# Kernel tuning notes

Measured on AMD Instinct MI355X. Metric: run time of the kernel, lower is better.

## Reference

```python
import jax, jax.numpy as jnp
import numpy as np

HEADS = 16
HEAD_DIM = 64
DIM = HEADS * HEAD_DIM          # 1024
TEXT_LEN = 226
N_CONCEPTS = 8
FRAMES = 4
PATCHES = 16 * 24               # H*W per latent frame
IMG_LEN = FRAMES * PATCHES      # 1536
TIME_DIM = 512
FF_DIM = 4 * DIM
TOPK_HEADS = 4                  # imap_sep_topk
LN_EPS = 1e-5
QK_EPS = 1e-6


def _layer_norm(x, w, b, eps):
    mu = jnp.mean(x, -1, keepdims=True)
    var = jnp.var(x, -1, keepdims=True)
    return (x - mu) * jax.lax.rsqrt(var + eps) * w + b


def _norm_zero(h, e, temb, lw, lb, nw, nb):
    # CogVideoXLayerNormZero: adaLN shift/scale/gate for hidden and encoder streams
    s = jax.nn.silu(temb) @ lw + lb                      # [B, 6*DIM]
    shift, scale, gate, e_shift, e_scale, e_gate = jnp.split(s, 6, axis=1)
    hn = _layer_norm(h, nw, nb, LN_EPS) * (1 + scale)[:, None] + shift[:, None]
    en = _layer_norm(e, nw, nb, LN_EPS) * (1 + e_scale)[:, None] + e_shift[:, None]
    return hn, en, gate[:, None], e_gate[:, None]


def _heads(x):
    B, S, _ = x.shape
    return x.reshape(B, S, HEADS, HEAD_DIM).transpose(0, 2, 1, 3)


def _rope(x, cos, sin):
    # diffusers apply_rotary_emb, use_real_unbind_dim=-1
    xr = x.reshape(*x.shape[:-1], HEAD_DIM // 2, 2)
    rot = jnp.stack([-xr[..., 1], xr[..., 0]], -1).reshape(x.shape)
    return x * cos + rot * sin


def _sdpa(q, k, v):
    s = jnp.einsum('bhqd,bhkd->bhqk', q, k) * (1.0 / np.sqrt(HEAD_DIM))
    return jnp.einsum('bhqk,bhkd->bhqd', jax.nn.softmax(s, -1), v)


def _attention(norm_h, norm_e, norm_c, rope_cos, rope_sin,
               wq, wk, wv, nq_w, nq_b, nk_w, nk_b, wo, bo):
    B = norm_h.shape[0]
    hs = jnp.concatenate([norm_e, norm_h], axis=1)       # [B, T+P, DIM]
    q, k, v = _heads(hs @ wq), _heads(hs @ wk), _heads(hs @ wv)
    cq, ck, cv = _heads(norm_c @ wq), _heads(norm_c @ wk), _heads(norm_c @ wv)
    q = _layer_norm(q, nq_w, nq_b, QK_EPS); cq = _layer_norm(cq, nq_w, nq_b, QK_EPS)
    k = _layer_norm(k, nk_w, nk_b, QK_EPS); ck = _layer_norm(ck, nk_w, nk_b, QK_EPS)
    q = q.at[:, :, TEXT_LEN:].set(_rope(q[:, :, TEXT_LEN:], rope_cos, rope_sin))
    k = k.at[:, :, TEXT_LEN:].set(_rope(k[:, :, TEXT_LEN:], rope_cos, rope_sin))

    attn_out = _sdpa(q, k, v)                            # [B,H,S,D]
    img_hidden = attn_out[:, :, TEXT_LEN:]               # [B,H,IMG_LEN,D]

    # select_head (reconstructed): per-head spread of image-token activations, top-k heads
    head_score = jnp.std(jnp.mean(img_hidden[1], -1), -1)        # [H]
    _, sel_head_idx = jax.lax.top_k(head_score, TOPK_HEADS)

    iq, ik, iv = q[:, :, TEXT_LEN:], k[:, :, TEXT_LEN:], v[:, :, TEXT_LEN:]
    cat_q = jnp.concatenate([cq, iq], 2)
    cat_k = jnp.concatenate([ck, ik], 2)
    cat_v = jnp.concatenate([cv, iv], 2)
    concept_attn = _sdpa(cat_q, cat_k, cat_v)
    attn_concept = concept_attn[:, :, :N_CONCEPTS]       # [B,H,C,D]

    cross_maps = jnp.mean(jnp.einsum('hpd,hcd->hcp', iq[1], ck[1]), axis=0)
    concept_maps = jnp.sum(jnp.einsum('hcd,hpd->hcp', attn_concept[1], img_hidden[1]), axis=0)

    # select_visual_token (reconstructed): per (head, concept, frame) argmax patch of q.k sim
    text_key = ck[1]                                      # imap_qk_matching_target == 'concept'
    sim = jnp.einsum('hpd,htd->htp', iq[1], text_key).reshape(HEADS, N_CONCEPTS, FRAMES, PATCHES)
    sel_vis_idx = jnp.argmax(sim, axis=-1)                # [H,T,F]

    img_r = img_hidden[1].reshape(HEADS, FRAMES, PATCHES, HEAD_DIM)
    h_ix = jnp.arange(HEADS)[:, None, None]
    f_ix = jnp.arange(FRAMES)[None, None, :]
    sel_img = img_r[h_ix, f_ix, sel_vis_idx]              # [H,T,F,D] gather
    imap = jnp.einsum('htfd,hfpd->htfp', sel_img, img_r)
    imap = (imap - imap.mean(1, keepdims=True)) / (jnp.std(imap, axis=1, keepdims=True, ddof=1) + 1e-6)
    imap = imap.reshape(HEADS, N_CONCEPTS, FRAMES * PATCHES)
    sel_imap = jnp.mean(imap[sel_head_idx], axis=0)       # [T, F*P]
    imap_sum = jnp.sum(imap, axis=0)

    def merge(x):
        return x.transpose(0, 2, 1, 3).reshape(B, x.shape[2], DIM)

    out = merge(attn_out) @ wo + bo
    c_out = merge(attn_concept) @ wo + bo
    return out[:, TEXT_LEN:], out[:, :TEXT_LEN], c_out, sel_imap, imap_sum, concept_maps, cross_maps


def _ff(x, w1, b1, w2, b2):
    return jax.nn.gelu(x @ w1 + b1, approximate=True) @ w2 + b2


def _block(hidden_states, encoder_hidden_states, concept_hidden_states, temb,
           rope_cos, rope_sin,
           norm1_w, norm1_b, ln1_w, ln1_b, norm2_w, norm2_b, ln2_w, ln2_b,
           wq, wk, wv, nq_w, nq_b, nk_w, nk_b, wo, bo,
           ff_w1, ff_b1, ff_w2, ff_b2):
    h, e, c = hidden_states, encoder_hidden_states, concept_hidden_states
    nh, ne, g_msa, eg_msa = _norm_zero(h, e, temb, norm1_w, norm1_b, ln1_w, ln1_b)
    _, nc, _, cg_msa = _norm_zero(h, c, temb, norm1_w, norm1_b, ln1_w, ln1_b)

    a_h, a_e, a_c, sel_imap, imap, concept_maps, cross_maps = _attention(
        nh, ne, nc, rope_cos, rope_sin, wq, wk, wv, nq_w, nq_b, nk_w, nk_b, wo, bo)

    h = h + g_msa * a_h
    e = e + eg_msa * a_e
    c = c + cg_msa * a_c

    nh, ne, g_ff, eg_ff = _norm_zero(h, e, temb, norm2_w, norm2_b, ln2_w, ln2_b)
    _, nc, _, cg_ff = _norm_zero(h, c, temb, norm2_w, norm2_b, ln2_w, ln2_b)

    ff_out = _ff(jnp.concatenate([ne, nh], axis=1), ff_w1, ff_b1, ff_w2, ff_b2)
    ff_c = _ff(nc, ff_w1, ff_b1, ff_w2, ff_b2)
    h = h + g_ff * ff_out[:, TEXT_LEN:]
    e = e + eg_ff * ff_out[:, :TEXT_LEN]
    c = c + cg_ff * ff_c
    return h, e, c, sel_imap, imap, concept_maps, cross_maps


def setup_inputs():
    key = jax.random.key(0)
    ks = jax.random.split(key, 16)
    p = lambda i, shape: jax.random.normal(ks[i], shape, jnp.float32) * 0.02
    return dict(
        hidden_states=jax.random.normal(ks[0], (2, IMG_LEN, DIM), jnp.float32),
        encoder_hidden_states=jax.random.normal(ks[1], (2, TEXT_LEN, DIM), jnp.float32),
        concept_hidden_states=jax.random.normal(ks[2], (2, N_CONCEPTS, DIM), jnp.float32),
        temb=jax.random.normal(ks[3], (2, TIME_DIM), jnp.float32),
        rope_cos=jax.random.uniform(ks[4], (IMG_LEN, HEAD_DIM), jnp.float32),
        rope_sin=jax.random.uniform(ks[5], (IMG_LEN, HEAD_DIM), jnp.float32),
        norm1_w=p(6, (TIME_DIM, 6 * DIM)), norm1_b=jnp.zeros((6 * DIM,), jnp.float32),
        ln1_w=jnp.ones((DIM,), jnp.float32), ln1_b=jnp.zeros((DIM,), jnp.float32),
        norm2_w=p(7, (TIME_DIM, 6 * DIM)), norm2_b=jnp.zeros((6 * DIM,), jnp.float32),
        ln2_w=jnp.ones((DIM,), jnp.float32), ln2_b=jnp.zeros((DIM,), jnp.float32),
        wq=p(8, (DIM, DIM)), wk=p(9, (DIM, DIM)), wv=p(10, (DIM, DIM)),
        nq_w=jnp.ones((HEAD_DIM,), jnp.float32), nq_b=jnp.zeros((HEAD_DIM,), jnp.float32),
        nk_w=jnp.ones((HEAD_DIM,), jnp.float32), nk_b=jnp.zeros((HEAD_DIM,), jnp.float32),
        wo=p(11, (DIM, DIM)), bo=jnp.zeros((DIM,), jnp.float32),
        ff_w1=p(12, (DIM, FF_DIM)), ff_b1=jnp.zeros((FF_DIM,), jnp.float32),
        ff_w2=p(13, (FF_DIM, DIM)), ff_b2=jnp.zeros((DIM,), jnp.float32),
    )


def reference(hidden_states, encoder_hidden_states, concept_hidden_states, temb,
              rope_cos, rope_sin,
              norm1_w, norm1_b, ln1_w, ln1_b, norm2_w, norm2_b, ln2_w, ln2_b,
              wq, wk, wv, nq_w, nq_b, nk_w, nk_b, wo, bo,
              ff_w1, ff_b1, ff_w2, ff_b2):
    return _block(hidden_states, encoder_hidden_states, concept_hidden_states, temb,
                  rope_cos, rope_sin,
                  norm1_w, norm1_b, ln1_w, ln1_b, norm2_w, norm2_b, ln2_w, ln2_b,
                  wq, wk, wv, nq_w, nq_b, nk_w, nk_b, wo, bo,
                  ff_w1, ff_b1, ff_w2, ff_b2)
```

## Files before the change

### kernel.cpp

```cpp
#include <hip/hip_runtime.h>
#include <hip/hip_bf16.h>
#include <math.h>

#define B_ 2
#define HEADS_ 16
#define HD_ 64
#define DIM_ 1024
#define TEXT_ 226
#define NC_ 8
#define FRAMES_ 4
#define PATCHES_ 384
#define IMG_ 1536
#define S_MAIN 1762
#define S2_ 1770
#define TD_ 512
#define FF_ 4096
#define ROWS_ (B_*S2_)
#define VPAD_ 1792

#define OFF_S1   0L
#define OFF_S2   12288L
#define OFF_MISC 24576L
#define OFF_SIM  25600L
#define OFF_IMAP 222208L
#define OFF_AC   418816L
#define OFF_X    435200L
#define OFF_PROJ 4060160L
#define OFF_XN   7685120L
#define OFF_Q    11310080L
#define OFF_K    14935040L
#define OFF_V    18560000L
#define OFF_AO   22184960L
#define OFF_XNB  25809920L

#define O_H    0L
#define O_E    3145728L
#define O_C    3608576L
#define O_SELI 3624960L
#define O_ISUM 3637248L
#define O_CMAP 3649536L
#define O_XMAP 3661824L

typedef __bf16 bf16x8_t __attribute__((ext_vector_type(8)));
typedef float  f32x4_t  __attribute__((ext_vector_type(4)));

__device__ __forceinline__ unsigned int pack2bf(float a, float b) {
    unsigned short ua = __builtin_bit_cast(unsigned short, (__bf16)a);
    unsigned short ub = __builtin_bit_cast(unsigned short, (__bf16)b);
    return (unsigned int)ua | ((unsigned int)ub << 16);
}

__device__ __forceinline__ void stage16(const unsigned short* g, unsigned short* l) {
    __builtin_amdgcn_global_load_lds(
        (const __attribute__((address_space(1))) unsigned int*)g,
        (__attribute__((address_space(3))) unsigned int*)l, 16, 0, 0);
}

__global__ __launch_bounds__(256) void k_silu_mod(
    const float* __restrict__ temb, const float* __restrict__ w1, const float* __restrict__ b1,
    const float* __restrict__ w2, const float* __restrict__ b2,
    float* __restrict__ s1, float* __restrict__ s2)
{
    int gout = blockIdx.x * 64 + (threadIdx.x & 63);
    int ks = threadIdx.x >> 6;
    int which = gout / 12288;
    int r = gout % 12288;
    int b = r / 6144, n = r % 6144;
    const float* w = which ? w2 : w1;
    const float* bb = which ? b2 : b1;
    const float* t = temb + b * TD_;
    float acc = 0.f;
    for (int k = ks*128; k < ks*128 + 128; ++k) {
        float tv = t[k];
        float sv = tv / (1.f + __expf(-tv));
        acc += sv * w[(long)k * 6144 + n];
    }
    __shared__ float red[256];
    red[threadIdx.x] = acc; __syncthreads();
    if (ks == 0) {
        int lt = threadIdx.x;
        float v = red[lt] + red[lt+64] + red[lt+128] + red[lt+192] + bb[n];
        (which ? s2 : s1)[b * 6144 + n] = v;
    }
}

__global__ __launch_bounds__(256) void k_tcvt(
    const float* __restrict__ src, unsigned short* __restrict__ dst, int K, int N)
{
    __shared__ float t[32][33];
    int n0 = blockIdx.x * 32, k0 = blockIdx.y * 32;
    int tx = threadIdx.x & 31, ty = threadIdx.x >> 5;
    #pragma unroll
    for (int i = 0; i < 4; ++i)
        t[ty + 8*i][tx] = src[(size_t)(k0 + ty + 8*i) * N + n0 + tx];
    __syncthreads();
    #pragma unroll
    for (int i = 0; i < 4; ++i) {
        float v = t[tx][ty + 8*i];
        dst[(size_t)(n0 + ty + 8*i) * K + k0 + tx] =
            __builtin_bit_cast(unsigned short, (__bf16)v);
    }
}

__global__ __launch_bounds__(256) void k_tcvt_qkv(
    const float* __restrict__ wq, const float* __restrict__ wk, const float* __restrict__ wv,
    unsigned short* __restrict__ dst)
{
    const float* src = (blockIdx.z == 0) ? wq : (blockIdx.z == 1) ? wk : wv;
    unsigned short* d = dst + (size_t)blockIdx.z * 1024 * 1024;
    __shared__ float t[32][33];
    int n0 = blockIdx.x * 32, k0 = blockIdx.y * 32;
    int tx = threadIdx.x & 31, ty = threadIdx.x >> 5;
    #pragma unroll
    for (int i = 0; i < 4; ++i)
        t[ty + 8*i][tx] = src[(size_t)(k0 + ty + 8*i) * 1024 + n0 + tx];
    __syncthreads();
    #pragma unroll
    for (int i = 0; i < 4; ++i) {
        float v = t[tx][ty + 8*i];
        d[(size_t)(n0 + ty + 8*i) * 1024 + k0 + tx] =
            __builtin_bit_cast(unsigned short, (__bf16)v);
    }
}

__global__ __launch_bounds__(256) void k_vtrans(
    const float* __restrict__ vh, unsigned short* __restrict__ vb)
{
    int bh = blockIdx.z;
    int d0 = blockIdx.y * 32;
    int s0 = blockIdx.x * 32;
    __shared__ float t[32][33];
    int tx = threadIdx.x & 31, ty = threadIdx.x >> 5;
    const float* src = vh + (size_t)bh * S2_ * 64;
    #pragma unroll
    for (int i = 0; i < 4; ++i) {
        int s = s0 + ty + 8*i; if (s >= S2_) s = S2_ - 1;
        t[ty + 8*i][tx] = src[(size_t)s*64 + d0 + tx];
    }
    __syncthreads();
    unsigned short* dst = vb + (size_t)bh * 64 * VPAD_;
    #pragma unroll
    for (int i = 0; i < 4; ++i) {
        int d = d0 + ty + 8*i;
        dst[(size_t)d * VPAD_ + s0 + tx] =
            __builtin_bit_cast(unsigned short, (__bf16)t[tx][ty + 8*i]);
    }
}

__global__ __launch_bounds__(256) void k_ln_mod(
    const float* pe, long bse, const float* ph, long bsh, const float* pc, long bsc,
    const float* __restrict__ smod, const float* __restrict__ lnw, const float* __restrict__ lnb,
    float* __restrict__ out, unsigned short* __restrict__ outb)
{
    long row = blockIdx.x;
    int b = (int)(row / S2_), s = (int)(row % S2_);
    const float* src; int shiftB, scaleB;
    if (s < TEXT_)       { src = pe + (long)b*bse + (long)s*DIM_;          shiftB = 3072; scaleB = 4096; }
    else if (s < S_MAIN) { src = ph + (long)b*bsh + (long)(s-TEXT_)*DIM_;  shiftB = 0;    scaleB = 1024; }
    else                 { src = pc + (long)b*bsc + (long)(s-S_MAIN)*DIM_; shiftB = 3072; scaleB = 4096; }
    int tid = threadIdx.x;
    int col = tid * 4;
    float4 x = *(const float4*)(src + col);
    float lsum = x.x + x.y + x.z + x.w;
    float lsq  = x.x*x.x + x.y*x.y + x.z*x.z + x.w*x.w;
    __shared__ float r1[256], r2[256];
    r1[tid] = lsum; r2[tid] = lsq; __syncthreads();
    for (int st = 128; st; st >>= 1) {
        if (tid < st) { r1[tid] += r1[tid+st]; r2[tid] += r2[tid+st]; }
        __syncthreads();
    }
    float mu = r1[0] * (1.f / DIM_);
    float var = r2[0] * (1.f / DIM_) - mu * mu;
    float rstd = rsqrtf(var + 1e-5f);
    const float* sb = smod + (long)b * 6144;
    float xs[4] = {x.x, x.y, x.z, x.w};
    float res[4];
    #pragma unroll
    for (int i = 0; i < 4; ++i) {
        int cc = col + i;
        float yy = (xs[i] - mu) * rstd * lnw[cc] + lnb[cc];
        res[i] = yy * (1.f + sb[scaleB + cc]) + sb[shiftB + cc];
    }
    if (out)
        *(float4*)(out + row * DIM_ + col) = make_float4(res[0], res[1], res[2], res[3]);
    uint2 pk;
    pk.x = pack2bf(res[0], res[1]); pk.y = pack2bf(res[2], res[3]);
    *(uint2*)(outb + row * DIM_ + col) = pk;
}

__global__ __launch_bounds__(256, 4) void k_bgemm(
    const unsigned short* __restrict__ A, const unsigned short* __restrict__ Wt,
    const float* __restrict__ bias, float* __restrict__ out_f,
    unsigned short* __restrict__ out_b, int M, int N, int K, int kz_len, int mode,
    float* __restrict__ q_out, float* __restrict__ k_out, float* __restrict__ v_out)
{
    __shared__ unsigned short at[2][128*32];
    __shared__ unsigned short bt[2][128*32];
    int tid = threadIdx.x;
    int w = tid >> 6, lane = tid & 63;
    int lr = lane & 15, lh = lane >> 4;
    int wm = w >> 1, wn = w & 1;
    int m0 = blockIdx.y * 128, n0 = blockIdx.x * 128;
    int kbeg = blockIdx.z * kz_len, kend = kbeg + kz_len;

    f32x4_t acc[4][4];
    #pragma unroll
    for (int i = 0; i < 4; ++i)
        #pragma unroll
        for (int j = 0; j < 4; ++j) { acc[i][j][0]=0.f; acc[i][j][1]=0.f; acc[i][j][2]=0.f; acc[i][j][3]=0.f; }

    int r4 = tid >> 2, c4 = tid & 3;
    int arow0 = m0 + r4;      if (arow0 >= M) arow0 = M - 1;
    int arow1 = m0 + 64 + r4; if (arow1 >= M) arow1 = M - 1;
    const unsigned short* ga0 = A + (size_t)arow0 * K + c4 * 8;
    const unsigned short* ga1 = A + (size_t)arow1 * K + c4 * 8;
    const unsigned short* gb0 = Wt + (size_t)(n0 + r4) * K + c4 * 8;
    const unsigned short* gb1 = Wt + (size_t)(n0 + 64 + r4) * K + c4 * 8;
    int lbase = w * 512;

    stage16(ga0 + kbeg, &at[0][lbase]);
    stage16(ga1 + kbeg, &at[0][lbase + 2048]);
    stage16(gb0 + kbeg, &bt[0][lbase]);
    stage16(gb1 + kbeg, &bt[0][lbase + 2048]);
    __syncthreads();
    int buf = 0;
    for (int k0 = kbeg; k0 < kend; k0 += 32) {
        bool more = (k0 + 32) < kend;
        if (more) {
            int nb = buf ^ 1;
            stage16(ga0 + k0 + 32, &at[nb][lbase]);
            stage16(ga1 + k0 + 32, &at[nb][lbase + 2048]);
            stage16(gb0 + k0 + 32, &bt[nb][lbase]);
            stage16(gb1 + k0 + 32, &bt[nb][lbase + 2048]);
        }
        int4 af[4], bf[4];
        #pragma unroll
        for (int tm = 0; tm < 4; ++tm)
            af[tm] = *(const int4*)&at[buf][(wm*64 + tm*16 + lr)*32 + lh*8];
        #pragma unroll
        for (int tn = 0; tn < 4; ++tn)
            bf[tn] = *(const int4*)&bt[buf][(wn*64 + tn*16 + lr)*32 + lh*8];
        #pragma unroll
        for (int tm = 0; tm < 4; ++tm) {
            bf16x8_t av = __builtin_bit_cast(bf16x8_t, af[tm]);
            #pragma unroll
            for (int tn = 0; tn < 4; ++tn)
                acc[tm][tn] = __builtin_amdgcn_mfma_f32_16x16x32_bf16(
                    av, __builtin_bit_cast(bf16x8_t, bf[tn]), acc[tm][tn], 0, 0, 0);
        }
        __syncthreads();
        buf ^= 1;
    }
    float* of = out_f;
    if (mode == 1) of += (size_t)blockIdx.z * M * N;
    #pragma unroll
    for (int tm = 0; tm < 4; ++tm) {
        #pragma unroll
        for (int r = 0; r < 4; ++r) {
            int m = m0 + wm*64 + tm*16 + lh*4 + r;
            if (m >= M) continue;
            int b = m / S2_, s = m % S2_;
            #pragma unroll
            for (int tn = 0; tn < 4; ++tn) {
                int n = n0 + wn*64 + tn*16 + lr;
                float v = acc[tm][tn][r];
                if (mode == 0) {
                    int which = n >> 10, c = n & 1023;
                    int hh = c >> 6, d = c & 63;
                    float* dstp = (which == 0) ? q_out : (which == 1) ? k_out : v_out;
                    dstp[(((size_t)b*HEADS_ + hh)*S2_ + s)*64 + d] = v;
                } else if (mode == 1) {
                    of[(size_t)m * N + n] = v + (bias ? bias[n] : 0.f);
                } else {
                    float x = v + bias[n];
                    float u = 0.7978845608028654f * (x + 0.044715f*x*x*x);
                    float g = x / (1.f + __expf(-2.f*u));
                    out_b[(size_t)m * N + n] = __builtin_bit_cast(unsigned short, (__bf16)g);
                }
            }
        }
    }
}

__global__ __launch_bounds__(256) void k_gemm(
    const float* __restrict__ A, const float* __restrict__ W,
    float* __restrict__ C, int M, int N, int K, int kz_len, int headed, int row_off,
    float* __restrict__ part)
{
    __shared__ float As[16][68];
    __shared__ float Bs[16][68];
    int tid = threadIdx.x;
    int bm = blockIdx.y * 64, bn = blockIdx.x * 64;
    int tr = tid >> 4, tc = tid & 15;
    int ar = tid >> 2, akk = (tid & 3) * 4;
    int bkk = tid >> 4, bn4 = (tid & 15) * 4;
    float acc[4][4] = {{0.f}};
    int garow = bm + ar;
    const float* Aptr = A + (size_t)garow * K + akk;
    const float* Wptr = W + (size_t)bkk * N + bn + bn4;
    int kbeg = blockIdx.z * kz_len;
    for (int k0 = kbeg; k0 < kbeg + kz_len; k0 += 16) {
        float4 av = make_float4(0.f, 0.f, 0.f, 0.f);
        if (garow < M) av = *(const float4*)(Aptr + k0);
        As[akk+0][ar] = av.x; As[akk+1][ar] = av.y; As[akk+2][ar] = av.z; As[akk+3][ar] = av.w;
        float4 bv = *(const float4*)(Wptr + (size_t)k0 * N);
        Bs[bkk][bn4+0] = bv.x; Bs[bkk][bn4+1] = bv.y; Bs[bkk][bn4+2] = bv.z; Bs[bkk][bn4+3] = bv.w;
        __syncthreads();
        #pragma unroll
        for (int kk = 0; kk < 16; ++kk) {
            float4 a = *(const float4*)&As[kk][tr*4];
            float4 bq = *(const float4*)&Bs[kk][tc*4];
            float avv[4] = {a.x, a.y, a.z, a.w};
            float bvv[4] = {bq.x, bq.y, bq.z, bq.w};
            #pragma unroll
            for (int i = 0; i < 4; ++i)
                #pragma unroll
                for (int j = 0; j < 4; ++j)
                    acc[i][j] += avv[i] * bvv[j];
        }
        __syncthreads();
    }
    #pragma unroll
    for (int i = 0; i < 4; ++i) {
        int r = bm + tr*4 + i;
        if (r >= M) continue;
        #pragma unroll
        for (int j = 0; j < 4; ++j) {
            int n = bn + tc*4 + j;
            float v = acc[i][j];
            if (part) {
                part[(size_t)blockIdx.z*M*N + (size_t)r*N + n] = v;
            } else if (headed) {
                int rg = r + row_off;
                int b = rg / S2_, s = rg % S2_;
                int hh = n >> 6, d = n & 63;
                C[(((size_t)b*HEADS_ + hh)*S2_ + s)*64 + d] = v;
            } else {
                C[(size_t)(r + row_off) * N + n] = v;
            }
        }
    }
}

__global__ __launch_bounds__(256) void k_fixred(
    const float* __restrict__ pa, float* __restrict__ qh_out)
{
    long i = (long)blockIdx.x*256 + threadIdx.x;
    int r = (int)(i >> 10), n = (int)(i & 1023);
    float v = pa[i] + pa[i + (long)IMG_*DIM_];
    int hh = n >> 6, d = n & 63;
    qh_out[(((size_t)HEADS_ + hh)*S2_ + TEXT_ + r)*64 + d] = v;
}

__global__ __launch_bounds__(256) void k_qk_prep(
    float* qh, float* kh, unsigned short* qbb, unsigned short* kbb,
    const float* __restrict__ nqw, const float* __restrict__ nqb,
    const float* __restrict__ nkw, const float* __restrict__ nkb,
    const float* __restrict__ rc, const float* __restrict__ rs)
{
    int which = blockIdx.y;
    int wid = threadIdx.x >> 6;
    int lane = threadIdx.x & 63;
    long row = (long)blockIdx.x * 4 + wid;
    long s = row % S2_;
    bool b1 = row >= (long)HEADS_*S2_;
    float* base = (which ? kh : qh) + row * 64;
    const float* w  = which ? nkw : nqw;
    const float* bb = which ? nkb : nqb;
    float x = base[lane];
    float sum = x;
    for (int off = 1; off < 64; off <<= 1) sum += __shfl_xor(sum, off, 64);
    float mu = sum * (1.f / 64.f);
    float dx = x - mu;
    float v = dx * dx;
    for (int off = 1; off < 64; off <<= 1) v += __shfl_xor(v, off, 64);
    float rstd = rsqrtf(v * (1.f / 64.f) + 1e-6f);
    float y = dx * rstd * w[lane] + bb[lane];
    if (s >= TEXT_ && s < S_MAIN) {
        long p = s - TEXT_;
        float part = __shfl_xor(y, 1, 64);
        float rot = (lane & 1) ? part : -part;
        y = y * rc[p*64 + lane] + rot * rs[p*64 + lane];
    }
    bool needf = b1 && (which ? (s >= S_MAIN) : (s >= TEXT_ && s < S_MAIN));
    if (needf) base[lane] = y;
    (which ? kbb : qbb)[row * 64 + lane] = __builtin_bit_cast(unsigned short, (__bf16)y);
}

__global__ __launch_bounds__(256) void k_flash(
    const unsigned short* __restrict__ qb, const unsigned short* __restrict__ kb,
    const unsigned short* __restrict__ vb,
    float* __restrict__ p0, float* __restrict__ p1, float* __restrict__ pl)
{
    int bx = blockIdx.x;
    int h = blockIdx.y, b = blockIdx.z;
    int qt, NQ, q_off, r0s, r0e, r1s, r1e, z;
    if (bx < 28) {
        z = bx & 1; int u = bx >> 1;
        qt = u*128; NQ = S_MAIN; q_off = 0;
        r0s = z ? 896 : 0; r0e = z ? S_MAIN : 896;
        r1s = 0; r1e = 0;
    } else {
        z = bx - 28;
        qt = 0; NQ = NC_; q_off = S_MAIN;
        if (z == 0) { r0s = S_MAIN;      r0e = S2_;    r1s = TEXT_; r1e = TEXT_ + 768; }
        else        { r0s = TEXT_ + 768; r0e = S_MAIN; r1s = 0;     r1e = 0; }
    }
    float* po = z ? p1 : p0;
    int tid = threadIdx.x;
    int w = tid >> 6, lane = tid & 63;
    int lr = lane & 15, lh = lane >> 4;
    __shared__ __align__(16) unsigned short kt[64*72];
    __shared__ __align__(16) unsigned short vt[64*72];
    __shared__ __align__(16) unsigned short pbuf[4*32*72];
    unsigned short* pw = pbuf + w*32*72;
    const unsigned short* qbase = qb + (((size_t)b*HEADS_ + h)*S2_ + q_off)*64;
    const unsigned short* kbase = kb + ((size_t)b*HEADS_ + h)*S2_*64;
    const unsigned short* vbase = vb + (size_t)(b*HEADS_ + h)*64*VPAD_;
    bf16x8_t aq[2][2];
    #pragma unroll
    for (int t = 0; t < 2; ++t) {
        int qrow = qt + w*32 + t*16 + lr; if (qrow >= NQ) qrow = NQ - 1;
        const unsigned short* qsrc = qbase + (size_t)qrow*64 + lh*8;
        aq[t][0] = __builtin_bit_cast(bf16x8_t, *(const int4*)qsrc);
        aq[t][1] = __builtin_bit_cast(bf16x8_t, *(const int4*)(qsrc + 32));
    }
    int4 onesi = make_int4(0x3F803F80, 0x3F803F80, 0x3F803F80, 0x3F803F80);
    bf16x8_t bones = __builtin_bit_cast(bf16x8_t, onesi);
    f32x4_t O[2][4];
    f32x4_t Lacc[2];
    #pragma unroll
    for (int t = 0; t < 2; ++t) {
        Lacc[t][0]=0.f; Lacc[t][1]=0.f; Lacc[t][2]=0.f; Lacc[t][3]=0.f;
        #pragma unroll
        for (int g = 0; g < 4; ++g) { O[t][g][0]=0.f; O[t][g][1]=0.f; O[t][g][2]=0.f; O[t][g][3]=0.f; }
    }
    for (int rgi = 0; rgi < 2; ++rgi) {
        int rs = rgi ? r1s : r0s, re = rgi ? r1e : r0e;
        for (int j0 = rs; j0 < re; j0 += 64) {
            int cnt = min(64, re - j0);
            __syncthreads();
            #pragma unroll
            for (int i = 0; i < 2; ++i) {
                int idx = tid + i*256;
                int key = idx >> 3, p8 = idx & 7;
                int krow = j0 + key; if (krow > re - 1) krow = re - 1;
                *(int4*)&kt[key*72 + p8*8] = *(const int4*)(kbase + (size_t)krow*64 + p8*8);
            }
            #pragma unroll
            for (int i = 0; i < 2; ++i) {
                int idx = tid + i*256;
                int d = idx >> 3, p8 = idx & 7;
                *(int4*)&vt[d*72 + p8*8] = *(const int4*)(vbase + (size_t)d*VPAD_ + j0 + p8*8);
            }
            __syncthreads();
            f32x4_t S[2][4];
            #pragma unroll
            for (int g = 0; g < 4; ++g) {
                const unsigned short* kr = &kt[(16*g + lr)*72 + lh*8];
                bf16x8_t b0 = __builtin_bit_cast(bf16x8_t, *(const int4*)kr);
                bf16x8_t b1 = __builtin_bit_cast(bf16x8_t, *(const int4*)(kr + 32));
                #pragma unroll
                for (int t = 0; t < 2; ++t) {
                    f32x4_t zz; zz[0]=0.f; zz[1]=0.f; zz[2]=0.f; zz[3]=0.f;
                    zz = __builtin_amdgcn_mfma_f32_16x16x32_bf16(aq[t][0], b0, zz, 0, 0, 0);
                    zz = __builtin_amdgcn_mfma_f32_16x16x32_bf16(aq[t][1], b1, zz, 0, 0, 0);
                    S[t][g] = zz;
                }
            }
            #pragma unroll
            for (int t = 0; t < 2; ++t)
                #pragma unroll
                for (int g = 0; g < 4; ++g) {
                    bool vld = (16*g + lr) < cnt;
                    #pragma unroll
                    for (int r = 0; r < 4; ++r) {
                        float p = vld ? __expf(S[t][g][r] * 0.125f) : 0.f;
                        pw[(t*16 + lh*4 + r)*72 + 16*g + lr] = __builtin_bit_cast(unsigned short, (__bf16)p);
                    }
                }
            #pragma unroll
            for (int c = 0; c < 2; ++c) {
                bf16x8_t ap[2];
                #pragma unroll
                for (int t = 0; t < 2; ++t) {
                    ap[t] = __builtin_bit_cast(bf16x8_t,
                        *(const int4*)&pw[(t*16 + lr)*72 + c*32 + lh*8]);
                    Lacc[t] = __builtin_amdgcn_mfma_f32_16x16x32_bf16(ap[t], bones, Lacc[t], 0, 0, 0);
                }
                #pragma unroll
                for (int g = 0; g < 4; ++g) {
                    bf16x8_t bv = __builtin_bit_cast(bf16x8_t,
                        *(const int4*)&vt[(16*g + lr)*72 + c*32 + lh*8]);
                    #pragma unroll
                    for (int t = 0; t < 2; ++t)
                        O[t][g] = __builtin_amdgcn_mfma_f32_16x16x32_bf16(ap[t], bv, O[t][g], 0, 0, 0);
                }
            }
        }
    }
    #pragma unroll
    for (int t = 0; t < 2; ++t)
        #pragma unroll
        for (int r = 0; r < 4; ++r) {
            int gq = qt + w*32 + t*16 + lh*4 + r;
            if (gq < NQ) {
                long rrow = (long)(b*HEADS_ + h)*S2_ + q_off + gq;
                float* o = po + rrow*64 + lr;
                #pragma unroll
                for (int g = 0; g < 4; ++g) o[16*g] = O[t][g][r];
                if (lr == 0) pl[(long)z*(B_*HEADS_*S2_) + rrow] = Lacc[t][r];
            }
        }
}

__global__ __launch_bounds__(256) void k_fcomb(
    const float* __restrict__ p0, const float* __restrict__ p1,
    const float* __restrict__ pl,
    float* __restrict__ ao, float* __restrict__ ac)
{
    long i = (long)blockIdx.x*256 + threadIdx.x;
    int d = (int)(i & 63);
    long rrow = i >> 6;
    int s = (int)(rrow % S2_);
    int bh = (int)(rrow / S2_);
    float l = pl[rrow] + pl[rrow + (long)B_*HEADS_*S2_];
    float v = (p0[i] + p1[i]) / l;
    if (s < S_MAIN) ao[((long)bh*S_MAIN + s)*64 + d] = v;
    else            ac[((long)bh*NC_ + (s - S_MAIN))*64 + d] = v;
}

__global__ __launch_bounds__(256) void k_head_score(const float* __restrict__ ao, float* __restrict__ score)
{
    int h = blockIdx.x, tid = threadIdx.x;
    const float* base = ao + (((long)HEADS_ + h)*S_MAIN + TEXT_)*64;
    float sA = 0.f, sB = 0.f;
    for (int p = tid; p < IMG_; p += 256) {
        const float* r = base + (long)p*64;
        float mm = 0.f;
        for (int d = 0; d < 64; d += 4) {
            float4 v = *(const float4*)(r + d);
            mm += v.x + v.y + v.z + v.w;
        }
        mm *= (1.f / 64.f);
        sA += mm; sB += mm*mm;
    }
    __shared__ float r1[256], r2[256];
    r1[tid] = sA; r2[tid] = sB; __syncthreads();
    for (int st = 128; st; st >>= 1) {
        if (tid < st) { r1[tid] += r1[tid+st]; r2[tid] += r2[tid+st]; }
        __syncthreads();
    }
    if (tid == 0) {
        float mean = r1[0] / IMG_, ms = r2[0] / IMG_;
        score[h] = sqrtf(fmaxf(ms - mean*mean, 0.f));
    }
}

__global__ void k_top4(const float* __restrict__ score, int* __restrict__ sel)
{
    if (threadIdx.x == 0 && blockIdx.x == 0) {
        int used = 0;
        for (int k = 0; k < 4; ++k) {
            float best = -INFINITY; int bi = 0;
            for (int h2 = 0; h2 < 16; ++h2) {
                if (used & (1 << h2)) continue;
                if (score[h2] > best) { best = score[h2]; bi = h2; }
            }
            used |= 1 << bi; sel[k] = bi;
        }
    }
}

__global__ __launch_bounds__(512) void k_sim(
    const float* __restrict__ qh, const float* __restrict__ kh,
    float* __restrict__ sim, int* __restrict__ selvis)
{
    int blk = blockIdx.x;
    int h = blk >> 5, t = (blk >> 2) & 7, f = blk & 3;
    int tid = threadIdx.x;
    __shared__ float ckv[64];
    if (tid < 64) ckv[tid] = kh[(((long)HEADS_ + h)*S2_ + S_MAIN + t)*64 + tid];
    __syncthreads();
    float val = -INFINITY; int idx = 0x7fffffff;
    if (tid < PATCHES_) {
        const float* qrow = qh + (((long)HEADS_ + h)*S2_ + TEXT_ + f*PATCHES_ + tid)*64;
        float acc = 0.f;
        for (int d = 0; d < 64; d += 4) {
            float4 qv = *(const float4*)(qrow + d);
            acc += qv.x*ckv[d] + qv.y*ckv[d+1] + qv.z*ckv[d+2] + qv.w*ckv[d+3];
        }
        sim[((long)h*NC_ + t)*IMG_ + f*PATCHES_ + tid] = acc;
        val = acc; idx = tid;
    }
    __shared__ float sv[512]; __shared__ int si[512];
    sv[tid] = val; si[tid] = idx; __syncthreads();
    for (int st = 256; st; st >>= 1) {
        if (tid < st) {
            float v2 = sv[tid+st]; int i2 = si[tid+st];
            if (v2 > sv[tid] || (v2 == sv[tid] && i2 < si[tid])) { sv[tid] = v2; si[tid] = i2; }
        }
        __syncthreads();
    }
    if (tid == 0) selvis[blk] = si[0];
}

__global__ __launch_bounds__(256) void k_cross(const float* __restrict__ sim, float* __restrict__ out)
{
    int i = blockIdx.x*256 + threadIdx.x;
    int c = i / IMG_, p = i % IMG_;
    float acc = 0.f;
    for (int h = 0; h < 16; ++h) acc += sim[((long)h*NC_ + c)*IMG_ + p];
    out[O_XMAP + i] = acc * (1.f / 16.f);
}

__global__ __launch_bounds__(256) void k_concept_maps(
    const float* __restrict__ ac, const float* __restrict__ ao, float* __restrict__ out)
{
    int i = blockIdx.x*256 + threadIdx.x;
    int c = i / IMG_, p = i % IMG_;
    float acc = 0.f;
    for (int h = 0; h < 16; ++h) {
        const float* a = ac + (((long)HEADS_ + h)*NC_ + c)*64;
        const float* g = ao + (((long)HEADS_ + h)*S_MAIN + TEXT_ + p)*64;
        for (int d = 0; d < 64; d += 4) {
            float4 av = *(const float4*)(a + d);
            float4 gv = *(const float4*)(g + d);
            acc += av.x*gv.x + av.y*gv.y + av.z*gv.z + av.w*gv.w;
        }
    }
    out[O_CMAP + i] = acc;
}

__global__ void k_imap_raw(const float* __restrict__ ao, const int* __restrict__ selvis,
                           float* __restrict__ imap)
{
    int blk = blockIdx.x;
    int h = blk >> 5, t = (blk >> 2) & 7, f = blk & 3;
    int tid = threadIdx.x;
    __shared__ float sel[64];
    int pstar = selvis[blk];
    if (tid < 64) sel[tid] = ao[(((long)HEADS_ + h)*S_MAIN + TEXT_ + f*PATCHES_ + pstar)*64 + tid];
    __syncthreads();
    const float* g = ao + (((long)HEADS_ + h)*S_MAIN + TEXT_ + f*PATCHES_ + tid)*64;
    float acc = 0.f;
    for (int d = 0; d < 64; d += 4) {
        float4 gv = *(const float4*)(g + d);
        acc += gv.x*sel[d] + gv.y*sel[d+1] + gv.z*sel[d+2] + gv.w*sel[d+3];
    }
    imap[((long)h*NC_ + t)*IMG_ + f*PATCHES_ + tid] = acc;
}

__global__ __launch_bounds__(256) void k_imap_norm(float* __restrict__ imap)
{
    int i = blockIdx.x*256 + threadIdx.x;
    int h = i / IMG_, fp = i % IMG_;
    float v[8]; float mu = 0.f;
    #pragma unroll
    for (int t = 0; t < 8; ++t) { v[t] = imap[((long)h*NC_ + t)*IMG_ + fp]; mu += v[t]; }
    mu *= 0.125f;
    float var = 0.f;
    #pragma unroll
    for (int t = 0; t < 8; ++t) var += (v[t]-mu)*(v[t]-mu);
    float sd = sqrtf(var * (1.f / 7.f));
    float inv = 1.f / (sd + 1e-6f);
    #pragma unroll
    for (int t = 0; t < 8; ++t) imap[((long)h*NC_ + t)*IMG_ + fp] = (v[t]-mu)*inv;
}

__global__ __launch_bounds__(256) void k_imap_reduce(
    const float* __restrict__ imap, const int* __restrict__ sel, float* __restrict__ out)
{
    int i = blockIdx.x*256 + threadIdx.x;
    int t = i / IMG_, fp = i % IMG_;
    float sum = 0.f;
    for (int h = 0; h < 16; ++h) sum += imap[((long)h*NC_ + t)*IMG_ + fp];
    float ss = 0.f;
    for (int k = 0; k < 4; ++k) { int h = sel[k]; ss += imap[((long)h*NC_ + t)*IMG_ + fp]; }
    out[O_ISUM + i] = sum;
    out[O_SELI + i] = ss * 0.25f;
}

__global__ __launch_bounds__(256) void k_merge(
    const float* __restrict__ ao, const float* __restrict__ ac, unsigned short* __restrict__ xo)
{
    long i = (long)blockIdx.x*256 + threadIdx.x;
    int col = (int)(i & 1023);
    long row = i >> 10;
    int b = (int)(row / S2_), s = (int)(row % S2_);
    int h = col >> 6, d = col & 63;
    float v;
    if (s < S_MAIN) v = ao[(((long)b*HEADS_ + h)*S_MAIN + s)*64 + d];
    else            v = ac[(((long)b*HEADS_ + h)*NC_ + (s - S_MAIN))*64 + d];
    xo[i] = __builtin_bit_cast(unsigned short, (__bf16)v);
}

__global__ __launch_bounds__(256) void k_residual1(
    const float* __restrict__ pe, const float* __restrict__ ph, const float* __restrict__ pc,
    const float* __restrict__ p0, const float* __restrict__ p1, const float* __restrict__ bo,
    const float* __restrict__ s1, float* __restrict__ X)
{
    long i = (long)blockIdx.x*256 + threadIdx.x;
    int col = (int)(i & 1023);
    long row = i >> 10;
    int b = (int)(row / S2_), s = (int)(row % S2_);
    const float* sb = s1 + (long)b * 6144;
    float orig, gate;
    if (s < TEXT_)       { orig = pe[((long)b*TEXT_ + s)*DIM_ + col];            gate = sb[5120 + col]; }
    else if (s < S_MAIN) { orig = ph[((long)b*IMG_ + (s-TEXT_))*DIM_ + col];     gate = sb[2048 + col]; }
    else                 { orig = pc[((long)b*NC_ + (s-S_MAIN))*DIM_ + col];     gate = sb[5120 + col]; }
    X[i] = orig + gate * (p0[i] + p1[i] + bo[col]);
}

__global__ __launch_bounds__(256) void k_final(
    const float* __restrict__ X, const float* __restrict__ f0, const float* __restrict__ f1,
    const float* __restrict__ fb2, const float* __restrict__ s2, float* __restrict__ out)
{
    long i = (long)blockIdx.x*256 + threadIdx.x;
    int col = (int)(i & 1023);
    long row = i >> 10;
    int b = (int)(row / S2_), s = (int)(row % S2_);
    const float* sb = s2 + (long)b * 6144;
    float gate; float* o;
    if (s < TEXT_)       { gate = sb[5120 + col]; o = out + O_E + ((long)b*TEXT_ + s)*DIM_ + col; }
    else if (s < S_MAIN) { gate = sb[2048 + col]; o = out + O_H + ((long)b*IMG_ + (s-TEXT_))*DIM_ + col; }
    else                 { gate = sb[5120 + col]; o = out + O_C + ((long)b*NC_ + (s-S_MAIN))*DIM_ + col; }
    *o = X[i] + gate * (f0[i] + f1[i] + fb2[col]);
}

extern "C" void kernel_launch(void* const* d_in, const int* in_sizes, int n_in,
                              void* d_out, int out_size, void* d_ws, size_t ws_size,
                              hipStream_t stream)
{
    (void)in_sizes; (void)n_in; (void)out_size; (void)ws_size;
    const float* h_in = (const float*)d_in[0];
    const float* e_in = (const float*)d_in[1];
    const float* c_in = (const float*)d_in[2];
    const float* temb = (const float*)d_in[3];
    const float* rcos = (const float*)d_in[4];
    const float* rsin = (const float*)d_in[5];
    const float* n1w  = (const float*)d_in[6];
    const float* n1b  = (const float*)d_in[7];
    const float* ln1w = (const float*)d_in[8];
    const float* ln1b = (const float*)d_in[9];
    const float* n2w  = (const float*)d_in[10];
    const float* n2b  = (const float*)d_in[11];
    const float* ln2w = (const float*)d_in[12];
    const float* ln2b = (const float*)d_in[13];
    const float* wq   = (const float*)d_in[14];
    const float* wk   = (const float*)d_in[15];
    const float* wv   = (const float*)d_in[16];
    const float* nqw  = (const float*)d_in[17];
    const float* nqb  = (const float*)d_in[18];
    const float* nkw  = (const float*)d_in[19];
    const float* nkb  = (const float*)d_in[20];
    const float* wo   = (const float*)d_in[21];
    const float* bo   = (const float*)d_in[22];
    const float* fw1  = (const float*)d_in[23];
    const float* fb1  = (const float*)d_in[24];
    const float* fw2  = (const float*)d_in[25];
    const float* fb2  = (const float*)d_in[26];

    float* ws  = (float*)d_ws;
    float* out = (float*)d_out;
    float* s1   = ws + OFF_S1;
    float* s2   = ws + OFF_S2;
    float* score  = ws + OFF_MISC;
    int*   selh   = (int*)(ws + OFF_MISC + 16);
    int*   selvis = (int*)(ws + OFF_MISC + 32);
    float* sim  = ws + OFF_SIM;
    float* imap = ws + OFF_IMAP;
    float* ac   = ws + OFF_AC;
    float* X    = ws + OFF_X;
    float* proj = ws + OFF_PROJ;
    float* xn   = ws + OFF_XN;
    float* qh   = ws + OFF_Q;
    float* kh   = ws + OFF_K;
    float* vh   = ws + OFF_V;
    float* ao   = ws + OFF_AO;
    float* ffo  = proj;
    float* fixp = ws + OFF_AO;
    unsigned short* xnb   = (unsigned short*)(ws + OFF_XNB);
    unsigned short* wqkvT = (unsigned short*)(ws + OFF_PROJ);
    unsigned short* vb    = (unsigned short*)(ws + OFF_PROJ);
    unsigned short* qbb   = (unsigned short*)(ws + OFF_X);
    unsigned short* kbb   = qbb + (size_t)B_*HEADS_*S2_*64;
    unsigned short* woT   = (unsigned short*)(ws + OFF_AO + 2000000);
    unsigned short* fw1T  = (unsigned short*)(ws + OFF_V);
    unsigned short* fw2T  = (unsigned short*)(ws + OFF_AO);
    unsigned short* ffh   = (unsigned short*)(ws + OFF_Q);
    float* fp0 = vh;
    float* fp1 = xn;
    float* fpl = sim;

    hipLaunchKernelGGL(k_silu_mod, dim3(384), dim3(256), 0, stream, temb, n1w, n1b, n2w, n2b, s1, s2);
    hipLaunchKernelGGL(k_tcvt_qkv, dim3(32, 32, 3), dim3(256), 0, stream, wq, wk, wv, wqkvT);
    hipLaunchKernelGGL(k_ln_mod, dim3(ROWS_), dim3(256), 0, stream,
        e_in, (long)TEXT_*DIM_, h_in, (long)IMG_*DIM_, c_in, (long)NC_*DIM_, s1, ln1w, ln1b, xn, xnb);
    hipLaunchKernelGGL(k_bgemm, dim3(24, 28, 1), dim3(256), 0, stream,
        xnb, wqkvT, (const float*)nullptr, (float*)nullptr, (unsigned short*)nullptr,
        ROWS_, 3072, 1024, 1024, 0, qh, kh, vh);
    hipLaunchKernelGGL(k_gemm, dim3(16, 24, 2), dim3(256), 0, stream,
        xn + (long)(S2_ + TEXT_)*DIM_, wq, (float*)nullptr, IMG_, DIM_, DIM_, 512, 0, 0, fixp);
    hipLaunchKernelGGL(k_fixred, dim3(6144), dim3(256), 0, stream, fixp, qh);
    hipLaunchKernelGGL(k_gemm, dim3(16, 1, 1), dim3(256), 0, stream,
        xn + (long)(S2_ + S_MAIN)*DIM_, wk, kh, NC_, DIM_, DIM_, 1024, 1, S2_ + S_MAIN, (float*)nullptr);
    hipLaunchKernelGGL(k_qk_prep, dim3(14160, 2), dim3(256), 0, stream,
        qh, kh, qbb, kbb, nqw, nqb, nkw, nkb, rcos, rsin);
    hipLaunchKernelGGL(k_vtrans, dim3(56, 2, 32), dim3(256), 0, stream, vh, vb);
    hipLaunchKernelGGL(k_flash, dim3(30, 16, 2), dim3(256), 0, stream,
        qbb, kbb, vb, fp0, fp1, fpl);
    hipLaunchKernelGGL(k_fcomb, dim3(14160), dim3(256), 0, stream, fp0, fp1, fpl, ao, ac);
    hipLaunchKernelGGL(k_head_score, dim3(16), dim3(256), 0, stream, ao, score);
    hipLaunchKernelGGL(k_top4, dim3(1), dim3(64), 0, stream, score, selh);
    hipLaunchKernelGGL(k_sim, dim3(512), dim3(512), 0, stream, qh, kh, sim, selvis);
    hipLaunchKernelGGL(k_cross, dim3(48), dim3(256), 0, stream, sim, out);
    hipLaunchKernelGGL(k_concept_maps, dim3(48), dim3(256), 0, stream, ac, ao, out);
    hipLaunchKernelGGL(k_imap_raw, dim3(512), dim3(384), 0, stream, ao, selvis, imap);
    hipLaunchKernelGGL(k_imap_norm, dim3(96), dim3(256), 0, stream, imap);
    hipLaunchKernelGGL(k_imap_reduce, dim3(48), dim3(256), 0, stream, imap, selh, out);
    hipLaunchKernelGGL(k_merge, dim3(14160), dim3(256), 0, stream, ao, ac, xnb);
    hipLaunchKernelGGL(k_tcvt, dim3(32, 32), dim3(256), 0, stream, wo, woT, 1024, 1024);
    hipLaunchKernelGGL(k_bgemm, dim3(8, 28, 2), dim3(256), 0, stream,
        xnb, woT, (const float*)nullptr, proj, (unsigned short*)nullptr, ROWS_, DIM_, 1024, 512, 1,
        (float*)nullptr, (float*)nullptr, (float*)nullptr);
    hipLaunchKernelGGL(k_residual1, dim3(14160), dim3(256), 0, stream,
        e_in, h_in, c_in, proj, proj + (size_t)ROWS_*DIM_, bo, s1, X);
    hipLaunchKernelGGL(k_tcvt, dim3(128, 32), dim3(256), 0, stream, fw1, fw1T, 1024, 4096);
    hipLaunchKernelGGL(k_tcvt, dim3(32, 128), dim3(256), 0, stream, fw2, fw2T, 4096, 1024);
    hipLaunchKernelGGL(k_ln_mod, dim3(ROWS_), dim3(256), 0, stream,
        X, (long)S2_*DIM_, X + (long)TEXT_*DIM_, (long)S2_*DIM_, X + (long)S_MAIN*DIM_, (long)S2_*DIM_,
        s2, ln2w, ln2b, (float*)nullptr, xnb);
    hipLaunchKernelGGL(k_bgemm, dim3(32, 28, 1), dim3(256), 0, stream,
        xnb, fw1T, fb1, (float*)nullptr, ffh, ROWS_, FF_, 1024, 1024, 2,
        (float*)nullptr, (float*)nullptr, (float*)nullptr);
    hipLaunchKernelGGL(k_bgemm, dim3(8, 28, 2), dim3(256), 0, stream,
        ffh, fw2T, (const float*)nullptr, ffo, (unsigned short*)nullptr, ROWS_, DIM_, FF_, 2048, 1,
        (float*)nullptr, (float*)nullptr, (float*)nullptr);
    hipLaunchKernelGGL(k_final, dim3(14160), dim3(256), 0, stream,
        X, ffo, ffo + (size_t)ROWS_*DIM_, fb2, s2, out);
}
```

Measured before the change: 734.4 us.

## Swizzle workgroups across XCDs, repad flash LDS, fuse merge into fcomb

Adds an XCD-aware workgroup remapping to the bf16 GEMM, fp32 GEMM and flash kernels so neighbouring tiles land on the same XCD and share L2. Changes the flash kernel's LDS row strides (K/V to 68, P to 76) to change bank-conflict behaviour, and adds a fast path that skips the validity mask when a key tile is full. Removes the separate k_merge kernel by having k_fcomb write the bf16 merged head layout directly, saving one launch and one fp32 re-read. The scattered bf16 writes in fcomb are strided and could be less coalesced than before.

```diff
diff --git a/kernel.cpp b/kernel.cpp
--- a/kernel.cpp
+++ b/kernel.cpp
@@ -41,6 +41,9 @@
 #define O_CMAP 3649536L
 #define O_XMAP 3661824L
 
+#define KS_ 68
+#define PS_ 76
+
 typedef __bf16 bf16x8_t __attribute__((ext_vector_type(8)));
 typedef float  f32x4_t  __attribute__((ext_vector_type(4)));
 
@@ -54,6 +57,11 @@
     __builtin_amdgcn_global_load_lds(
         (const __attribute__((address_space(1))) unsigned int*)g,
         (__attribute__((address_space(3))) unsigned int*)l, 16, 0, 0);
+}
+
+__device__ __forceinline__ int xcd_swz(int lin, int nwg) {
+    if ((nwg & 7) == 0) { int q = nwg >> 3; lin = (lin & 7) * q + (lin >> 3); }
+    return lin;
 }
 
 __global__ __launch_bounds__(256) void k_silu_mod(
@@ -200,7 +208,9 @@
     int w = tid >> 6, lane = tid & 63;
     int lr = lane & 15, lh = lane >> 4;
     int wm = w >> 1, wn = w & 1;
-    int m0 = blockIdx.y * 128, n0 = blockIdx.x * 128;
+    int gx = gridDim.x;
+    int lin = xcd_swz(blockIdx.y * gx + blockIdx.x, gx * gridDim.y);
+    int m0 = (lin / gx) * 128, n0 = (lin % gx) * 128;
     int kbeg = blockIdx.z * kz_len, kend = kbeg + kz_len;
 
     f32x4_t acc[4][4];
@@ -290,7 +300,9 @@
     __shared__ float As[16][68];
     __shared__ float Bs[16][68];
     int tid = threadIdx.x;
-    int bm = blockIdx.y * 64, bn = blockIdx.x * 64;
+    int gx = gridDim.x;
+    int lin = xcd_swz(blockIdx.y * gx + blockIdx.x, gx * gridDim.y);
+    int bm = (lin / gx) * 64, bn = (lin % gx) * 64;
     int tr = tid >> 4, tc = tid & 15;
     int ar = tid >> 2, akk = (tid & 3) * 4;
     int bkk = tid >> 4, bn4 = (tid & 15) * 4;
@@ -392,8 +404,11 @@
     const unsigned short* __restrict__ vb,
     float* __restrict__ p0, float* __restrict__ p1, float* __restrict__ pl)
 {
-    int bx = blockIdx.x;
-    int h = blockIdx.y, b = blockIdx.z;
+    int lin3 = (blockIdx.z * gridDim.y + blockIdx.y) * gridDim.x + blockIdx.x;
+    lin3 = xcd_swz(lin3, gridDim.x * gridDim.y * gridDim.z);
+    int bx = lin3 % 30;
+    int rest = lin3 / 30;
+    int h = rest & 15, b = rest >> 4;
     int qt, NQ, q_off, r0s, r0e, r1s, r1e, z;
     if (bx < 28) {
         z = bx & 1; int u = bx >> 1;
@@ -410,10 +425,10 @@
     int tid = threadIdx.x;
     int w = tid >> 6, lane = tid & 63;
     int lr = lane & 15, lh = lane >> 4;
-    __shared__ __align__(16) unsigned short kt[64*72];
-    __shared__ __align__(16) unsigned short vt[64*72];
-    __shared__ __align__(16) unsigned short pbuf[4*32*72];
-    unsigned short* pw = pbuf + w*32*72;
+    __shared__ __align__(16) unsigned short kt[64*KS_];
+    __shared__ __align__(16) unsigned short vt[64*KS_];
+    __shared__ __align__(16) unsigned short pbuf[4*32*PS_];
+    unsigned short* pw = pbuf + w*32*PS_;
     const unsigned short* qbase = qb + (((size_t)b*HEADS_ + h)*S2_ + q_off)*64;
     const unsigned short* kbase = kb + ((size_t)b*HEADS_ + h)*S2_*64;
     const unsigned short* vbase = vb + (size_t)(b*HEADS_ + h)*64*VPAD_;
@@ -445,19 +460,19 @@
                 int idx = tid + i*256;
                 int key = idx >> 3, p8 = idx & 7;
                 int krow = j0 + key; if (krow > re - 1) krow = re - 1;
-                *(int4*)&kt[key*72 + p8*8] = *(const int4*)(kbase + (size_t)krow*64 + p8*8);
+                *(int4*)&kt[key*KS_ + p8*8] = *(const int4*)(kbase + (size_t)krow*64 + p8*8);
             }
             #pragma unroll
             for (int i = 0; i < 2; ++i) {
                 int idx = tid + i*256;
                 int d = idx >> 3, p8 = idx & 7;
-                *(int4*)&vt[d*72 + p8*8] = *(const int4*)(vbase + (size_t)d*VPAD_ + j0 + p8*8);
+                *(int4*)&vt[d*KS_ + p8*8] = *(const int4*)(vbase + (size_t)d*VPAD_ + j0 + p8*8);
             }
             __syncthreads();
             f32x4_t S[2][4];
             #pragma unroll
             for (int g = 0; g < 4; ++g) {
-                const unsigned short* kr = &kt[(16*g + lr)*72 + lh*8];
+                const unsigned short* kr = &kt[(16*g + lr)*KS_ + lh*8];
                 bf16x8_t b0 = __builtin_bit_cast(bf16x8_t, *(const int4*)kr);
                 bf16x8_t b1 = __builtin_bit_cast(bf16x8_t, *(const int4*)(kr + 32));
                 #pragma unroll
@@ -468,30 +483,42 @@
                     S[t][g] = zz;
                 }
             }
-            #pragma unroll
-            for (int t = 0; t < 2; ++t)
+            if (cnt == 64) {
                 #pragma unroll
-                for (int g = 0; g < 4; ++g) {
-                    bool vld = (16*g + lr) < cnt;
+                for (int t = 0; t < 2; ++t)
                     #pragma unroll
-                    for (int r = 0; r < 4; ++r) {
-                        float p = vld ? __expf(S[t][g][r] * 0.125f) : 0.f;
-                        pw[(t*16 + lh*4 + r)*72 + 16*g + lr] = __builtin_bit_cast(unsigned short, (__bf16)p);
+                    for (int g = 0; g < 4; ++g)
+                        #pragma unroll
+                        for (int r = 0; r < 4; ++r) {
+                            float p = __expf(S[t][g][r] * 0.125f);
+                            pw[(t*16 + lh*4 + r)*PS_ + 16*g + lr] = __builtin_bit_cast(unsigned short, (__bf16)p);
+                        }
+            } else {
+                #pragma unroll
+                for (int t = 0; t < 2; ++t)
+                    #pragma unroll
+                    for (int g = 0; g < 4; ++g) {
+                        bool vld = (16*g + lr) < cnt;
+                        #pragma unroll
+                        for (int r = 0; r < 4; ++r) {
+                            float p = vld ? __expf(S[t][g][r] * 0.125f) : 0.f;
+                            pw[(t*16 + lh*4 + r)*PS_ + 16*g + lr] = __builtin_bit_cast(unsigned short, (__bf16)p);
+                        }
                     }
-                }
+            }
             #pragma unroll
             for (int c = 0; c < 2; ++c) {
                 bf16x8_t ap[2];
                 #pragma unroll
                 for (int t = 0; t < 2; ++t) {
                     ap[t] = __builtin_bit_cast(bf16x8_t,
-                        *(const int4*)&pw[(t*16 + lr)*72 + c*32 + lh*8]);
+                        *(const int4*)&pw[(t*16 + lr)*PS_ + c*32 + lh*8]);
                     Lacc[t] = __builtin_amdgcn_mfma_f32_16x16x32_bf16(ap[t], bones, Lacc[t], 0, 0, 0);
                 }
                 #pragma unroll
                 for (int g = 0; g < 4; ++g) {
                     bf16x8_t bv = __builtin_bit_cast(bf16x8_t,
-                        *(const int4*)&vt[(16*g + lr)*72 + c*32 + lh*8]);
+                        *(const int4*)&vt[(16*g + lr)*KS_ + c*32 + lh*8]);
                     #pragma unroll
                     for (int t = 0; t < 2; ++t)
                         O[t][g] = __builtin_amdgcn_mfma_f32_16x16x32_bf16(ap[t], bv, O[t][g], 0, 0, 0);
@@ -517,17 +544,19 @@
 __global__ __launch_bounds__(256) void k_fcomb(
     const float* __restrict__ p0, const float* __restrict__ p1,
     const float* __restrict__ pl,
-    float* __restrict__ ao, float* __restrict__ ac)
+    float* __restrict__ ao, float* __restrict__ ac, unsigned short* __restrict__ xo)
 {
     long i = (long)blockIdx.x*256 + threadIdx.x;
     int d = (int)(i & 63);
     long rrow = i >> 6;
     int s = (int)(rrow % S2_);
     int bh = (int)(rrow / S2_);
+    int b = bh >> 4, h = bh & 15;
     float l = pl[rrow] + pl[rrow + (long)B_*HEADS_*S2_];
     float v = (p0[i] + p1[i]) / l;
     if (s < S_MAIN) ao[((long)bh*S_MAIN + s)*64 + d] = v;
     else            ac[((long)bh*NC_ + (s - S_MAIN))*64 + d] = v;
+    xo[((long)b*S2_ + s)*DIM_ + h*64 + d] = __builtin_bit_cast(unsigned short, (__bf16)v);
 }
 
 __global__ __launch_bounds__(256) void k_head_score(const float* __restrict__ ao, float* __restrict__ score)
@@ -679,20 +708,6 @@
     for (int k = 0; k < 4; ++k) { int h = sel[k]; ss += imap[((long)h*NC_ + t)*IMG_ + fp]; }
     out[O_ISUM + i] = sum;
     out[O_SELI + i] = ss * 0.25f;
-}
-
-__global__ __launch_bounds__(256) void k_merge(
-    const float* __restrict__ ao, const float* __restrict__ ac, unsigned short* __restrict__ xo)
-{
-    long i = (long)blockIdx.x*256 + threadIdx.x;
-    int col = (int)(i & 1023);
-    long row = i >> 10;
-    int b = (int)(row / S2_), s = (int)(row % S2_);
-    int h = col >> 6, d = col & 63;
-    float v;
-    if (s < S_MAIN) v = ao[(((long)b*HEADS_ + h)*S_MAIN + s)*64 + d];
-    else            v = ac[(((long)b*HEADS_ + h)*NC_ + (s - S_MAIN))*64 + d];
-    xo[i] = __builtin_bit_cast(unsigned short, (__bf16)v);
 }
 
 __global__ __launch_bounds__(256) void k_residual1(
@@ -810,7 +825,7 @@
     hipLaunchKernelGGL(k_vtrans, dim3(56, 2, 32), dim3(256), 0, stream, vh, vb);
     hipLaunchKernelGGL(k_flash, dim3(30, 16, 2), dim3(256), 0, stream,
         qbb, kbb, vb, fp0, fp1, fpl);
-    hipLaunchKernelGGL(k_fcomb, dim3(14160), dim3(256), 0, stream, fp0, fp1, fpl, ao, ac);
+    hipLaunchKernelGGL(k_fcomb, dim3(14160), dim3(256), 0, stream, fp0, fp1, fpl, ao, ac, xnb);
     hipLaunchKernelGGL(k_head_score, dim3(16), dim3(256), 0, stream, ao, score);
     hipLaunchKernelGGL(k_top4, dim3(1), dim3(64), 0, stream, score, selh);
     hipLaunchKernelGGL(k_sim, dim3(512), dim3(512), 0, stream, qh, kh, sim, selvis);
@@ -819,7 +834,6 @@
     hipLaunchKernelGGL(k_imap_raw, dim3(512), dim3(384), 0, stream, ao, selvis, imap);
     hipLaunchKernelGGL(k_imap_norm, dim3(96), dim3(256), 0, stream, imap);
     hipLaunchKernelGGL(k_imap_reduce, dim3(48), dim3(256), 0, stream, imap, selh, out);
-    hipLaunchKernelGGL(k_merge, dim3(14160), dim3(256), 0, stream, ao, ac, xnb);
     hipLaunchKernelGGL(k_tcvt, dim3(32, 32), dim3(256), 0, stream, wo, woT, 1024, 1024);
     hipLaunchKernelGGL(k_bgemm, dim3(8, 28, 2), dim3(256), 0, stream,
         xnb, woT, (const float*)nullptr, proj, (unsigned short*)nullptr, ROWS_, DIM_, 1024, 512, 1,
```

After: 770.6 us. +4.9%, slower.
